# Optimization experiments

Hardware: AMD Instinct MI355X
Metric: run time of the kernel (lower is better)

The kernel has to match this reference:

```python
import jax, jax.numpy as jnp
import numpy as np

N0, N1 = 4096, 16384
HID, LAT, DIM, OUT = 128, 64, 3, 3
OFFS = [1, 2, 3, 5, 8]  # circulant graph offsets; A+A^3 support is offset sums


def _ring_edges(N, offs):
    # edge_index of A + A^3 for circulant adjacency with given offsets
    o = np.asarray(offs)
    s3 = (o[:, None, None] + o[None, :, None] + o[None, None, :]).ravel()
    aug = np.unique(np.concatenate([o, s3]))
    src = np.repeat(np.arange(N), aug.size)
    dst = (src + np.tile(aug, N)) % N
    return np.stack([src, dst]).astype(np.int32)


def _gatv2(x, src, dst, eattr, Wl, bl, Wr, br, We, att, bias, N):
    # PyG GATv2Conv, heads=1, add_self_loops=True with fill_value='mean'
    cnt = jax.ops.segment_sum(jnp.ones_like(dst, jnp.float32), dst, N)
    loop_attr = jax.ops.segment_sum(eattr, dst, N) / jnp.maximum(cnt, 1.0)[:, None]
    loops = jnp.arange(N, dtype=src.dtype)
    s = jnp.concatenate([src, loops])
    d = jnp.concatenate([dst, loops])
    ea = jnp.concatenate([eattr, loop_attr], 0)
    xl = x @ Wl.T + bl
    xr = x @ Wr.T + br
    m = xl[s] + xr[d] + ea @ We.T              # [E+N, HID]
    m = jnp.where(m > 0, m, 0.2 * m)           # leaky_relu(0.2)
    a = m @ att                                # [E+N]
    amax = jax.ops.segment_max(a, d, N)
    ex = jnp.exp(a - amax[d])
    den = jax.ops.segment_sum(ex, d, N)
    alpha = ex / (den[d] + 1e-16)
    return jax.ops.segment_sum(xl[s] * alpha[:, None], d, N) + bias


def _knn_interp(x, pos_x, pos_y, k=3):
    # PyG knn_interpolate: inverse-squared-distance weighted k-NN average
    d2 = (jnp.sum(pos_y ** 2, 1)[:, None] + jnp.sum(pos_x ** 2, 1)[None, :]
          - 2.0 * pos_y @ pos_x.T)             # [Ny, Nx]
    neg, idx = jax.lax.top_k(-d2, k)
    w = 1.0 / jnp.maximum(-neg, 1e-16)          # [Ny, k]
    return jnp.sum(x[idx] * w[..., None], 1) / jnp.sum(w, 1)[:, None]


def _forward(latent, pos0, pos1, eidx0, eidx1, conv_Wl, conv_bl, conv_Wr,
             conv_br, conv_We, conv_att, conv_bias, lin0_W, lin0_b, lins_W,
             lins_b, out_W, out_b):
    x = latent @ lin0_W.T + lin0_b
    src0, dst0 = eidx0[0], eidx0[1]
    ea0 = pos0[dst0] - pos0[src0]
    for c in (0, 1):
        h = jnp.concatenate([x, pos0], 1)
        x = jax.nn.elu(_gatv2(h, src0, dst0, ea0, conv_Wl[c], conv_bl[c],
                              conv_Wr[c], conv_br[c], conv_We[c], conv_att[c],
                              conv_bias[c], N0)) + h @ lins_W[c].T + lins_b[c]
    x = _knn_interp(x, pos0, pos1, 3)
    src1, dst1 = eidx1[0], eidx1[1]
    ea1 = pos1[dst1] - pos1[src1]
    for c in (2, 3):
        h = jnp.concatenate([x, pos1], 1)
        x = jax.nn.elu(_gatv2(h, src1, dst1, ea1, conv_Wl[c], conv_bl[c],
                              conv_Wr[c], conv_br[c], conv_We[c], conv_att[c],
                              conv_bias[c], N1)) + h @ lins_W[c].T + lins_b[c]
    h = jnp.concatenate([x, pos1], 1)
    return h @ out_W.T + out_b


def setup_inputs() -> dict:
    key = jax.random.key(0)
    ks = jax.random.split(key, 16)
    n = lambda i, shape, s=0.05: jax.random.normal(ks[i], shape, jnp.float32) * s
    IN = HID + DIM
    return dict(
        latent=jax.random.normal(ks[0], (N0, LAT), jnp.float32),
        pos0=jax.random.normal(ks[1], (N0, DIM), jnp.float32),
        pos1=jax.random.normal(ks[2], (N1, DIM), jnp.float32),
        eidx0=jnp.asarray(_ring_edges(N0, OFFS)),
        eidx1=jnp.asarray(_ring_edges(N1, OFFS)),
        conv_Wl=n(3, (4, HID, IN)), conv_bl=n(4, (4, HID)),
        conv_Wr=n(5, (4, HID, IN)), conv_br=n(6, (4, HID)),
        conv_We=n(7, (4, HID, DIM)), conv_att=n(8, (4, HID)),
        conv_bias=n(9, (4, HID)),
        lin0_W=n(10, (HID, LAT)), lin0_b=n(11, (HID,)),
        lins_W=n(12, (4, HID, IN)), lins_b=n(13, (4, HID)),
        out_W=n(14, (OUT, IN)), out_b=n(15, (OUT,)))


def reference(latent, pos0, pos1, eidx0, eidx1, conv_Wl, conv_bl, conv_Wr,
              conv_br, conv_We, conv_att, conv_bias, lin0_W, lin0_b, lins_W,
              lins_b, out_W, out_b):
    return _forward(latent, pos0, pos1, eidx0, eidx1, conv_Wl, conv_bl,
                    conv_Wr, conv_br, conv_We, conv_att, conv_bias, lin0_W,
                    lin0_b, lins_W, lins_b, out_W, out_b)
```

## Files before the change

kernel.cpp:

```cpp
#include <hip/hip_runtime.h>
#include <hip/hip_bf16.h>

#define N0 4096
#define N1 16384
#define HID 128
#define LAT 64
#define DIM 3
#define NAUG 21
#define JTOT 512
#define NG 5

typedef __attribute__((ext_vector_type(8))) short bf16x8;
typedef __attribute__((ext_vector_type(4))) float f32x4;

__device__ __constant__ int c_aug[NAUG] = {1,2,3,4,5,6,7,8,9,10,11,12,13,14,
                                           15,16,17,18,19,21,24};

__device__ __forceinline__ unsigned short f2bf(float v) {
    __hip_bfloat16 b = __float2bfloat16(v);
    return *reinterpret_cast<unsigned short*>(&b);
}

#define KCH 64
#define KCS 64
#define YPT 4
#define KNN_BLOCKS 1024

#define WSWZ_PER_LAYER 81920
#define H0G4 131072
#define H1G4 524288
#define PREP_BLOCKS 3880

__global__ __launch_bounds__(256)
void prep_knn_kernel(const float* __restrict__ Wl,
                     const float* __restrict__ Wr,
                     const float* __restrict__ We,
                     const float* __restrict__ linsW,
                     const float* __restrict__ bl,
                     const float* __restrict__ br,
                     const float* __restrict__ linsb,
                     const float* __restrict__ lin0W,
                     const float* __restrict__ pos0,
                     const float* __restrict__ pos1,
                     unsigned short* __restrict__ Wswz,
                     float* __restrict__ bias_cat,
                     float* __restrict__ Wt0,
                     unsigned short* __restrict__ hswz0A,
                     unsigned short* __restrict__ hswz0B,
                     unsigned short* __restrict__ hswz1A,
                     unsigned short* __restrict__ hswz1B,
                     float* __restrict__ pb_d,
                     int* __restrict__ pb_i) {
    __shared__ float4 sx[KCS];

    if (blockIdx.x < KNN_BLOCKS) {
        int tid = threadIdx.x;
        int chunk = blockIdx.x >> 4;
        int xpart = blockIdx.x & 15;
        if (tid < KCS) {
            const float* p = &pos0[(chunk * KCS + tid) * 3];
            float x = p[0], y = p[1], z = p[2];
            sx[tid] = make_float4(x, y, z, x * x + y * y + z * z);
        }
        __syncthreads();
        int ybase = xpart * (256 * YPT) + tid;
        float m2y[YPT][3], sy[YPT];
#pragma unroll
        for (int u = 0; u < YPT; ++u) {
            int y = ybase + u * 256;
            float p0 = pos1[y * 3], p1 = pos1[y * 3 + 1], p2 = pos1[y * 3 + 2];
            m2y[u][0] = -2.0f * p0; m2y[u][1] = -2.0f * p1; m2y[u][2] = -2.0f * p2;
            sy[u] = p0 * p0 + p1 * p1 + p2 * p2;
        }
        float bd0[YPT], bd1[YPT], bd2[YPT];
        int   bi0[YPT], bi1[YPT], bi2[YPT];
#pragma unroll
        for (int u = 0; u < YPT; ++u) {
            bd0[u] = 1e30f; bd1[u] = 1e30f; bd2[u] = 1e30f;
            bi0[u] = 0; bi1[u] = 0; bi2[u] = 0;
        }
        int gbase = chunk * KCS;
#pragma unroll 4
        for (int i = 0; i < KCS; i += 4) {
            float4 s[4];
#pragma unroll
            for (int v = 0; v < 4; ++v) s[v] = sx[i + v];
#pragma unroll
            for (int v = 0; v < 4; ++v) {
                int gi = gbase + i + v;
#pragma unroll
                for (int u = 0; u < YPT; ++u) {
                    float t = fmaf(m2y[u][0], s[v].x, s[v].w);
                    t = fmaf(m2y[u][1], s[v].y, t);
                    t = fmaf(m2y[u][2], s[v].z, t);
                    t += sy[u];
                    bool c0 = t < bd0[u];
                    bool c1 = t < bd1[u];
                    bool c2 = t < bd2[u];
                    float n0 = fminf(bd0[u], t);
                    float n1 = __builtin_amdgcn_fmed3f(bd0[u], bd1[u], t);
                    float n2 = __builtin_amdgcn_fmed3f(bd1[u], bd2[u], t);
                    int j0 = c0 ? gi : bi0[u];
                    int j1 = c0 ? bi0[u] : (c1 ? gi : bi1[u]);
                    int j2 = c1 ? bi1[u] : (c2 ? gi : bi2[u]);
                    bd0[u] = n0; bd1[u] = n1; bd2[u] = n2;
                    bi0[u] = j0; bi1[u] = j1; bi2[u] = j2;
                }
            }
        }
#pragma unroll
        for (int u = 0; u < YPT; ++u) {
            int y = ybase + u * 256;
            int base = (chunk * N1 + y) * 3;
            pb_d[base] = bd0[u]; pb_d[base + 1] = bd1[u]; pb_d[base + 2] = bd2[u];
            pb_i[base] = bi0[u]; pb_i[base + 1] = bi1[u]; pb_i[base + 2] = bi2[u];
        }
        return;
    }

    int tid = (blockIdx.x - KNN_BLOCKS) * blockDim.x + threadIdx.x;
    const int NSWZ = 4 * WSWZ_PER_LAYER;
    const int B0 = NSWZ;
    const int B1 = B0 + 4 * JTOT;
    const int B2 = B1 + 64 * 128;
    const int B3 = B2 + H0G4;
    const int B4 = B3 + H1G4;
    if (tid < NSWZ) {
        int c = tid / WSWZ_PER_LAYER;
        int r = tid - c * WSWZ_PER_LAYER;
        int nt = r / 2560;
        int g  = (r / 512) % 5;
        int l  = (r / 8) % 64;
        int j  = r % 8;
        int k  = g * 32 + (l >> 4) * 8 + j;
        int n  = nt * 16 + (l & 15);
        float v = 0.0f;
        if (k < 131) {
            if (n < 128)      v = Wl[(c * 128 + n) * 131 + k];
            else if (n < 256) v = Wr[(c * 128 + (n - 128)) * 131 + k];
            else if (n < 384) v = linsW[(c * 128 + (n - 256)) * 131 + k];
            else              v = (k >= 128) ? We[(c * 128 + (n - 384)) * 3 + (k - 128)]
                                             : 0.0f;
        }
        Wswz[tid] = f2bf(v);
    } else if (tid < B1) {
        int idx = tid - B0;
        int c = idx / JTOT;
        int j = idx - c * JTOT;
        float v;
        if (j < 128)        v = bl[c * 128 + j];
        else if (j < 256)   v = br[c * 128 + (j - 128)];
        else if (j < 384)   v = linsb[c * 128 + (j - 256)];
        else                v = 0.0f;
        bias_cat[idx] = v;
    } else if (tid < B2) {
        int idx = tid - B1;
        int k = idx / 128;
        int j = idx - k * 128;
        Wt0[idx] = lin0W[j * 64 + k];
    } else if (tid < B3) {
        int r = tid - B2;
        int j = r & 7;
        int l = (r >> 3) & 63;
        int mt = r >> 9;
        int row = mt * 16 + (l & 15);
        int k = 128 + (l >> 4) * 8 + j;
        float v = (k < 131) ? pos0[row * 3 + (k - 128)] : 0.0f;
        unsigned short bv = f2bf(v);
        size_t idx = (size_t)((mt * 5 + 4) * 64 + l) * 8 + j;
        hswz0A[idx] = bv;
        hswz0B[idx] = bv;
    } else if (tid < B4) {
        int r = tid - B3;
        int j = r & 7;
        int l = (r >> 3) & 63;
        int mt = r >> 9;
        int row = mt * 16 + (l & 15);
        int k = 128 + (l >> 4) * 8 + j;
        float v = (k < 131) ? pos1[row * 3 + (k - 128)] : 0.0f;
        unsigned short bv = f2bf(v);
        size_t idx = (size_t)((mt * 5 + 4) * 64 + l) * 8 + j;
        hswz1A[idx] = bv;
        hswz1B[idx] = bv;
    }
}

#define MERGE_BLOCKS 128

__global__ __launch_bounds__(128)
void lin0_merge_kernel(const float* __restrict__ latent,
                       const float* __restrict__ Wt0,
                       const float* __restrict__ b,
                       unsigned short* __restrict__ hswz0,
                       const float* __restrict__ pb_d,
                       const int* __restrict__ pb_i,
                       int* __restrict__ knn_idx,
                       float* __restrict__ knn_w) {
    __shared__ float lrow[64];

    if (blockIdx.x < MERGE_BLOCKS) {
        int y = blockIdx.x * 128 + threadIdx.x;
        float bd0 = 1e30f, bd1 = 1e30f, bd2 = 1e30f;
        int bi0 = 0, bi1 = 0, bi2 = 0;
        for (int c = 0; c < KCH; ++c) {
            int base = (c * N1 + y) * 3;
#pragma unroll
            for (int t3 = 0; t3 < 3; ++t3) {
                float t = pb_d[base + t3];
                int gi = pb_i[base + t3];
                bool c0 = t < bd0;
                bool c1 = t < bd1;
                bool c2 = t < bd2;
                float n0 = fminf(bd0, t);
                float n1 = __builtin_amdgcn_fmed3f(bd0, bd1, t);
                float n2 = __builtin_amdgcn_fmed3f(bd1, bd2, t);
                int j0 = c0 ? gi : bi0;
                int j1 = c0 ? bi0 : (c1 ? gi : bi1);
                int j2 = c1 ? bi1 : (c2 ? gi : bi2);
                bd0 = n0; bd1 = n1; bd2 = n2;
                bi0 = j0; bi1 = j1; bi2 = j2;
            }
        }
        knn_idx[y * 3]     = bi0;
        knn_idx[y * 3 + 1] = bi1;
        knn_idx[y * 3 + 2] = bi2;
        knn_w[y * 3]     = 1.0f / fmaxf(bd0, 1e-16f);
        knn_w[y * 3 + 1] = 1.0f / fmaxf(bd1, 1e-16f);
        knn_w[y * 3 + 2] = 1.0f / fmaxf(bd2, 1e-16f);
        return;
    }

    int n = blockIdx.x - MERGE_BLOCKS;
    int j = threadIdx.x;
    if (j < 64) lrow[j] = latent[n * 64 + j];
    __syncthreads();
    float acc = b[j];
#pragma unroll 8
    for (int k = 0; k < 64; ++k) acc += lrow[k] * Wt0[k * 128 + j];
    int g = j >> 5, sub = (j >> 3) & 3, jj = j & 7;
    hswz0[(size_t)(((n >> 4) * 5 + g) * 64 + sub * 16 + (n & 15)) * 8 + jj] = f2bf(acc);
}

#define WROW 40
#define FSTR 132
__global__ __launch_bounds__(512, 2)
void fused_layer_kernel(const unsigned short* __restrict__ hswz,
                        const unsigned short* __restrict__ Wswz,
                        const float* __restrict__ bias_cat,
                        const float* __restrict__ att,
                        const float* __restrict__ bias,
                        float* __restrict__ linb,
                        float* __restrict__ xout,
                        unsigned short* __restrict__ hout,
                        const float* __restrict__ outW,
                        const float* __restrict__ outb,
                        const float* __restrict__ pos1,
                        int mode, int N) {
    __shared__ float xls_s[WROW][FSTR];
    __shared__ float pes_s[WROW][FSTR];
    __shared__ float xr_s[16][FSTR];

    int tid = threadIdx.x;
    int w = tid >> 6;
    int l = tid & 63;
    int quad = l >> 4, lcol = l & 15;
    int mt0 = blockIdx.x;
    int n0 = mt0 * 16;
    int MT = N >> 4;

    bf16x8 a[3][NG];
#pragma unroll
    for (int i = 0; i < 3; ++i) {
        int mt = mt0 - 2 + i;
        if (mt < 0) mt += MT;
#pragma unroll
        for (int g = 0; g < NG; ++g)
            a[i][g] = *(const bf16x8*)&hswz[(size_t)((mt * NG + g) * 64 + l) * 8];
    }

#pragma unroll
    for (int i = 0; i < 4; ++i) {
        int b = i * 8 + w;
        int colbase = (b & 7) * 16;
        int ntw, kind;
        if (b < 8)       { ntw = b;      kind = 0; }
        else if (b < 16) { ntw = 16 + b; kind = 1; }
        else if (b < 24) { ntw = b - 8;  kind = 2; }
        else             { ntw = b - 8;  kind = 3; }
        bf16x8 bf[NG];
#pragma unroll
        for (int g = 0; g < NG; ++g)
            bf[g] = *(const bf16x8*)&Wswz[(size_t)((ntw * NG + g) * 64 + l) * 8];
        float bv = bias_cat[ntw * 16 + lcol];
        if (kind < 2) {
            float (*dst)[FSTR] = (kind == 0) ? xls_s : pes_s;
#pragma unroll
            for (int m = 0; m < 3; ++m) {
                f32x4 c = {bv, bv, bv, bv};
#pragma unroll
                for (int g = 0; g < NG; ++g)
                    c = __builtin_amdgcn_mfma_f32_16x16x32_bf16(a[m][g], bf[g], c, 0, 0, 0);
                if (m == 0) {
                    if (quad >= 2) {
                        int w0 = (quad - 2) * 4;
#pragma unroll
                        for (int r = 0; r < 4; ++r) dst[w0 + r][colbase + lcol] = c[r];
                    }
                } else {
                    int w0 = m * 16 - 8 + quad * 4;
#pragma unroll
                    for (int r = 0; r < 4; ++r) dst[w0 + r][colbase + lcol] = c[r];
                }
            }
        } else if (kind == 2) {
            f32x4 c = {bv, bv, bv, bv};
#pragma unroll
            for (int g = 0; g < NG; ++g)
                c = __builtin_amdgcn_mfma_f32_16x16x32_bf16(a[2][g], bf[g], c, 0, 0, 0);
            int w0 = quad * 4;
#pragma unroll
            for (int r = 0; r < 4; ++r) xr_s[w0 + r][colbase + lcol] = c[r];
        } else {
            f32x4 c = {bv, bv, bv, bv};
#pragma unroll
            for (int g = 0; g < NG; ++g)
                c = __builtin_amdgcn_mfma_f32_16x16x32_bf16(a[2][g], bf[g], c, 0, 0, 0);
            int jj = colbase + lcol;
#pragma unroll
            for (int r = 0; r < 4; ++r)
                linb[(size_t)(n0 + quad * 4 + r) * 128 + jj] = c[r];
        }
    }
    __syncthreads();

    int qh = l >> 5;
    int t = l & 31;
    int dl = w * 2 + qh;
    int d = n0 + dl;
    int selfrow = dl + 24;
    int i0 = t * 4;

    f32x4 linv = *(const f32x4*)&linb[(size_t)d * 128 + i0];

    float att4[4], base[4], xld[4], pesum[4], o[4];
    {
        f32x4 a0 = *(const f32x4*)&att[i0];
        f32x4 r0 = *(const f32x4*)&xr_s[dl][i0];
        f32x4 x0 = *(const f32x4*)&xls_s[selfrow][i0];
        f32x4 p0 = *(const f32x4*)&pes_s[selfrow][i0];
#pragma unroll
        for (int j = 0; j < 4; ++j) {
            att4[j] = a0[j];
            xld[j]  = x0[j];
            base[j] = r0[j] + p0[j];
            pesum[j] = 0.0f;
            o[j] = 0.0f;
        }
    }

    float den = 0.0f;

#pragma unroll
    for (int k = 0; k < NAUG; ++k) {
        int lr = selfrow - c_aug[k];
        float xls[4], pes[4];
        *(f32x4*)&xls[0] = *(const f32x4*)&xls_s[lr][i0];
        *(f32x4*)&pes[0] = *(const f32x4*)&pes_s[lr][i0];
        float p = 0.0f;
#pragma unroll
        for (int j = 0; j < 4; ++j) {
            float mm = xls[j] + base[j] - pes[j];
            mm = mm > 0.0f ? mm : 0.2f * mm;
            p = fmaf(att4[j], mm, p);
            pesum[j] += pes[j];
        }
        p += __shfl_xor(p, 1, 64);
        p += __shfl_xor(p, 2, 64);
        p += __shfl_xor(p, 4, 64);
        p += __shfl_xor(p, 8, 64);
        p += __shfl_xor(p, 16, 64);
        float wgt = __expf(p);
        den += wgt;
#pragma unroll
        for (int j = 0; j < 4; ++j) o[j] = fmaf(wgt, xls[j], o[j]);
    }
    {
        const float inv21 = 1.0f / 21.0f;
        float p = 0.0f;
#pragma unroll
        for (int j = 0; j < 4; ++j) {
            float mm = xld[j] + base[j] - pesum[j] * inv21;
            mm = mm > 0.0f ? mm : 0.2f * mm;
            p = fmaf(att4[j], mm, p);
        }
        p += __shfl_xor(p, 1, 64);
        p += __shfl_xor(p, 2, 64);
        p += __shfl_xor(p, 4, 64);
        p += __shfl_xor(p, 8, 64);
        p += __shfl_xor(p, 16, 64);
        float wgt = __expf(p);
        den += wgt;
#pragma unroll
        for (int j = 0; j < 4; ++j) o[j] = fmaf(wgt, xld[j], o[j]);
    }

    float inv = 1.0f / (den + 1e-16f);
    float res[4];
    {
        f32x4 b0 = *(const f32x4*)&bias[i0];
#pragma unroll
        for (int j = 0; j < 4; ++j) {
            float v = o[j] * inv + b0[j];
            v = v > 0.0f ? v : __expf(v) - 1.0f;
            res[j] = v + linv[j];
        }
    }

    if (mode == 0) {
        *(f32x4*)&xout[(size_t)d * 128 + i0] = *(f32x4*)&res[0];
    } else if (mode == 1) {
        unsigned short ob[4];
#pragma unroll
        for (int j = 0; j < 4; ++j) ob[j] = f2bf(res[j]);
        int g = i0 >> 5, sub = (i0 >> 3) & 3, jj = i0 & 7;
        *(uint2*)&hout[(size_t)((((d >> 4) * 5 + g) * 64) + sub * 16 + (d & 15)) * 8 + jj]
            = *(uint2*)ob;
    } else {
        float po[3];
#pragma unroll
        for (int o3 = 0; o3 < 3; ++o3) {
            const float* wr = &outW[o3 * 131 + i0];
            float p = res[0] * wr[0];
            p = fmaf(res[1], wr[1], p);
            p = fmaf(res[2], wr[2], p);
            p = fmaf(res[3], wr[3], p);
            p += __shfl_xor(p, 1, 64);
            p += __shfl_xor(p, 2, 64);
            p += __shfl_xor(p, 4, 64);
            p += __shfl_xor(p, 8, 64);
            p += __shfl_xor(p, 16, 64);
            po[o3] = p;
        }
        if (t == 0) {
            float p0 = pos1[d * 3], p1 = pos1[d * 3 + 1], p2 = pos1[d * 3 + 2];
#pragma unroll
            for (int o3 = 0; o3 < 3; ++o3) {
                xout[d * 3 + o3] = po[o3] + outb[o3] + p0 * outW[o3 * 131 + 128]
                                 + p1 * outW[o3 * 131 + 129] + p2 * outW[o3 * 131 + 130];
            }
        }
    }
}

__global__ __launch_bounds__(256)
void interp_kernel(const float* __restrict__ x0, const int* __restrict__ knn_idx,
                   const float* __restrict__ knn_w, unsigned short* __restrict__ hswz) {
    int wave = threadIdx.x >> 6;
    int lane = threadIdx.x & 63;
    int y = blockIdx.x * 4 + wave;
    int i0 = 2 * lane;
    float w0 = knn_w[y * 3], w1 = knn_w[y * 3 + 1], w2 = knn_w[y * 3 + 2];
    int j0 = knn_idx[y * 3], j1 = knn_idx[y * 3 + 1], j2 = knn_idx[y * 3 + 2];
    float inv = 1.0f / (w0 + w1 + w2);
    float2 a = *(const float2*)&x0[(size_t)j0 * 128 + i0];
    float2 b = *(const float2*)&x0[(size_t)j1 * 128 + i0];
    float2 c = *(const float2*)&x0[(size_t)j2 * 128 + i0];
    float rx = (w0 * a.x + w1 * b.x + w2 * c.x) * inv;
    float ry = (w0 * a.y + w1 * b.y + w2 * c.y) * inv;
    unsigned int packed = (unsigned int)f2bf(rx) | ((unsigned int)f2bf(ry) << 16);
    int g = i0 >> 5, sub = (i0 >> 3) & 3, jj = i0 & 7;
    size_t idx = (size_t)((((y >> 4) * 5 + g) * 64) + sub * 16 + (y & 15)) * 8 + jj;
    *(unsigned int*)&hswz[idx] = packed;
}

extern "C" void kernel_launch(void* const* d_in, const int* in_sizes, int n_in,
                              void* d_out, int out_size, void* d_ws, size_t ws_size,
                              hipStream_t stream) {
    (void)in_sizes; (void)n_in; (void)out_size; (void)ws_size;
    const float* latent   = (const float*)d_in[0];
    const float* pos0     = (const float*)d_in[1];
    const float* pos1     = (const float*)d_in[2];
    const float* conv_Wl  = (const float*)d_in[5];
    const float* conv_bl  = (const float*)d_in[6];
    const float* conv_Wr  = (const float*)d_in[7];
    const float* conv_br  = (const float*)d_in[8];
    const float* conv_We  = (const float*)d_in[9];
    const float* conv_att = (const float*)d_in[10];
    const float* conv_bias= (const float*)d_in[11];
    const float* lin0_W   = (const float*)d_in[12];
    const float* lin0_b   = (const float*)d_in[13];
    const float* lins_W   = (const float*)d_in[14];
    const float* lins_b   = (const float*)d_in[15];
    const float* out_W    = (const float*)d_in[16];
    const float* out_b    = (const float*)d_in[17];
    float* out = (float*)d_out;

    char* ws = (char*)d_ws;
    unsigned short* Wswz = (unsigned short*)ws; ws += (size_t)4 * WSWZ_PER_LAYER * 2;
    float* bias_cat = (float*)ws;  ws += (size_t)4 * JTOT * 4;
    float* Wt0      = (float*)ws;  ws += (size_t)64 * 128 * 4;
    unsigned short* hswz0A = (unsigned short*)ws; ws += (size_t)(N0 / 16) * NG * 64 * 8 * 2;
    unsigned short* hswz0B = (unsigned short*)ws; ws += (size_t)(N0 / 16) * NG * 64 * 8 * 2;
    unsigned short* hswz1A = (unsigned short*)ws; ws += (size_t)(N1 / 16) * NG * 64 * 8 * 2;
    unsigned short* hswz1B = (unsigned short*)ws; ws += (size_t)(N1 / 16) * NG * 64 * 8 * 2;
    float* bufA     = (float*)ws;  ws += (size_t)N0 * 128 * 4;
    float* linb     = (float*)ws;  ws += (size_t)N1 * 128 * 4;
    float* pb_d     = (float*)ws;  ws += (size_t)KCH * N1 * 3 * 4;
    int*   pb_i     = (int*)ws;    ws += (size_t)KCH * N1 * 3 * 4;
    int*   knn_idx  = (int*)ws;    ws += (size_t)N1 * 3 * 4;
    float* knn_w    = (float*)ws;  ws += (size_t)N1 * 3 * 4;

    prep_knn_kernel<<<KNN_BLOCKS + PREP_BLOCKS, 256, 0, stream>>>(
        conv_Wl, conv_Wr, conv_We, lins_W, conv_bl, conv_br, lins_b, lin0_W,
        pos0, pos1, Wswz, bias_cat, Wt0, hswz0A, hswz0B, hswz1A, hswz1B,
        pb_d, pb_i);

    lin0_merge_kernel<<<MERGE_BLOCKS + N0, 128, 0, stream>>>(
        latent, Wt0, lin0_b, hswz0A, pb_d, pb_i, knn_idx, knn_w);

    fused_layer_kernel<<<N0 / 16, 512, 0, stream>>>(
        hswz0A, Wswz + (size_t)0 * WSWZ_PER_LAYER, bias_cat + 0 * JTOT,
        conv_att + 0 * 128, conv_bias + 0 * 128, linb, nullptr, hswz0B,
        nullptr, nullptr, nullptr, 1, N0);
    fused_layer_kernel<<<N0 / 16, 512, 0, stream>>>(
        hswz0B, Wswz + (size_t)1 * WSWZ_PER_LAYER, bias_cat + 1 * JTOT,
        conv_att + 1 * 128, conv_bias + 1 * 128, linb, bufA, nullptr,
        nullptr, nullptr, nullptr, 0, N0);

    interp_kernel<<<N1 / 4, 256, 0, stream>>>(bufA, knn_idx, knn_w, hswz1A);

    fused_layer_kernel<<<N1 / 16, 512, 0, stream>>>(
        hswz1A, Wswz + (size_t)2 * WSWZ_PER_LAYER, bias_cat + 2 * JTOT,
        conv_att + 2 * 128, conv_bias + 2 * 128, linb, nullptr, hswz1B,
        nullptr, nullptr, nullptr, 1, N1);
    fused_layer_kernel<<<N1 / 16, 512, 0, stream>>>(
        hswz1B, Wswz + (size_t)3 * WSWZ_PER_LAYER, bias_cat + 3 * JTOT,
        conv_att + 3 * 128, conv_bias + 3 * 128, linb, out, nullptr,
        out_W, out_b, pos1, 2, N1);
}
```

Before: 235.1 us.

## Fold lin0 into prep kernel and kNN merge into first GAT layer

Moves the lin0 projection into the prep/kNN launch, reading lin0_W directly instead of a transposed Wt0 copy, and drops the separate Wt0 transpose. The kNN partial-merge blocks now ride alongside the first GATv2 layer's blocks in one launch, with the layer body factored into a shared device function. Together these remove one kernel launch and its serialization gap, and let the merge overlap with layer-0 work. The trade-off is that lin0 now uses uncoalesced per-thread row reads of the weights. Merge blocks use 512 threads under the layer kernel's launch bounds, which could affect occupancy.

```diff
diff --git a/kernel.cpp b/kernel.cpp
--- a/kernel.cpp
+++ b/kernel.cpp
@@ -29,28 +29,35 @@
 #define WSWZ_PER_LAYER 81920
 #define H0G4 131072
 #define H1G4 524288
-#define PREP_BLOCKS 3880
+#define P_NSWZ (4 * WSWZ_PER_LAYER)
+#define P_B0 P_NSWZ
+#define P_B1 (P_B0 + 4 * JTOT)
+#define P_B2 (P_B1 + H0G4)
+#define P_B3 (P_B2 + H1G4)
+#define PREP_BLOCKS (P_B3 / 256)
+#define LIN0_BLOCKS 2048
 
 __global__ __launch_bounds__(256)
-void prep_knn_kernel(const float* __restrict__ Wl,
-                     const float* __restrict__ Wr,
-                     const float* __restrict__ We,
-                     const float* __restrict__ linsW,
-                     const float* __restrict__ bl,
-                     const float* __restrict__ br,
-                     const float* __restrict__ linsb,
-                     const float* __restrict__ lin0W,
-                     const float* __restrict__ pos0,
-                     const float* __restrict__ pos1,
-                     unsigned short* __restrict__ Wswz,
-                     float* __restrict__ bias_cat,
-                     float* __restrict__ Wt0,
-                     unsigned short* __restrict__ hswz0A,
-                     unsigned short* __restrict__ hswz0B,
-                     unsigned short* __restrict__ hswz1A,
-                     unsigned short* __restrict__ hswz1B,
-                     float* __restrict__ pb_d,
-                     int* __restrict__ pb_i) {
+void prep_knn_lin0_kernel(const float* __restrict__ Wl,
+                          const float* __restrict__ Wr,
+                          const float* __restrict__ We,
+                          const float* __restrict__ linsW,
+                          const float* __restrict__ bl,
+                          const float* __restrict__ br,
+                          const float* __restrict__ linsb,
+                          const float* __restrict__ lin0W,
+                          const float* __restrict__ lin0b,
+                          const float* __restrict__ latent,
+                          const float* __restrict__ pos0,
+                          const float* __restrict__ pos1,
+                          unsigned short* __restrict__ Wswz,
+                          float* __restrict__ bias_cat,
+                          unsigned short* __restrict__ hswz0A,
+                          unsigned short* __restrict__ hswz0B,
+                          unsigned short* __restrict__ hswz1A,
+                          unsigned short* __restrict__ hswz1B,
+                          float* __restrict__ pb_d,
+                          int* __restrict__ pb_i) {
     __shared__ float4 sx[KCS];
 
     if (blockIdx.x < KNN_BLOCKS) {
@@ -118,131 +125,285 @@
         return;
     }
 
-    int tid = (blockIdx.x - KNN_BLOCKS) * blockDim.x + threadIdx.x;
-    const int NSWZ = 4 * WSWZ_PER_LAYER;
-    const int B0 = NSWZ;
-    const int B1 = B0 + 4 * JTOT;
-    const int B2 = B1 + 64 * 128;
-    const int B3 = B2 + H0G4;
-    const int B4 = B3 + H1G4;
-    if (tid < NSWZ) {
-        int c = tid / WSWZ_PER_LAYER;
-        int r = tid - c * WSWZ_PER_LAYER;
-        int nt = r / 2560;
-        int g  = (r / 512) % 5;
-        int l  = (r / 8) % 64;
-        int j  = r % 8;
-        int k  = g * 32 + (l >> 4) * 8 + j;
-        int n  = nt * 16 + (l & 15);
-        float v = 0.0f;
-        if (k < 131) {
-            if (n < 128)      v = Wl[(c * 128 + n) * 131 + k];
-            else if (n < 256) v = Wr[(c * 128 + (n - 128)) * 131 + k];
-            else if (n < 384) v = linsW[(c * 128 + (n - 256)) * 131 + k];
-            else              v = (k >= 128) ? We[(c * 128 + (n - 384)) * 3 + (k - 128)]
-                                             : 0.0f;
-        }
-        Wswz[tid] = f2bf(v);
-    } else if (tid < B1) {
-        int idx = tid - B0;
-        int c = idx / JTOT;
-        int j = idx - c * JTOT;
-        float v;
-        if (j < 128)        v = bl[c * 128 + j];
-        else if (j < 256)   v = br[c * 128 + (j - 128)];
-        else if (j < 384)   v = linsb[c * 128 + (j - 256)];
-        else                v = 0.0f;
-        bias_cat[idx] = v;
-    } else if (tid < B2) {
-        int idx = tid - B1;
-        int k = idx / 128;
-        int j = idx - k * 128;
-        Wt0[idx] = lin0W[j * 64 + k];
-    } else if (tid < B3) {
-        int r = tid - B2;
-        int j = r & 7;
-        int l = (r >> 3) & 63;
-        int mt = r >> 9;
-        int row = mt * 16 + (l & 15);
-        int k = 128 + (l >> 4) * 8 + j;
-        float v = (k < 131) ? pos0[row * 3 + (k - 128)] : 0.0f;
-        unsigned short bv = f2bf(v);
-        size_t idx = (size_t)((mt * 5 + 4) * 64 + l) * 8 + j;
-        hswz0A[idx] = bv;
-        hswz0B[idx] = bv;
-    } else if (tid < B4) {
-        int r = tid - B3;
-        int j = r & 7;
-        int l = (r >> 3) & 63;
-        int mt = r >> 9;
-        int row = mt * 16 + (l & 15);
-        int k = 128 + (l >> 4) * 8 + j;
-        float v = (k < 131) ? pos1[row * 3 + (k - 128)] : 0.0f;
-        unsigned short bv = f2bf(v);
-        size_t idx = (size_t)((mt * 5 + 4) * 64 + l) * 8 + j;
-        hswz1A[idx] = bv;
-        hswz1B[idx] = bv;
-    }
-}
-
-#define MERGE_BLOCKS 128
-
-__global__ __launch_bounds__(128)
-void lin0_merge_kernel(const float* __restrict__ latent,
-                       const float* __restrict__ Wt0,
-                       const float* __restrict__ b,
-                       unsigned short* __restrict__ hswz0,
-                       const float* __restrict__ pb_d,
-                       const int* __restrict__ pb_i,
-                       int* __restrict__ knn_idx,
-                       float* __restrict__ knn_w) {
-    __shared__ float lrow[64];
-
-    if (blockIdx.x < MERGE_BLOCKS) {
-        int y = blockIdx.x * 128 + threadIdx.x;
-        float bd0 = 1e30f, bd1 = 1e30f, bd2 = 1e30f;
-        int bi0 = 0, bi1 = 0, bi2 = 0;
-        for (int c = 0; c < KCH; ++c) {
-            int base = (c * N1 + y) * 3;
-#pragma unroll
-            for (int t3 = 0; t3 < 3; ++t3) {
-                float t = pb_d[base + t3];
-                int gi = pb_i[base + t3];
-                bool c0 = t < bd0;
-                bool c1 = t < bd1;
-                bool c2 = t < bd2;
-                float n0 = fminf(bd0, t);
-                float n1 = __builtin_amdgcn_fmed3f(bd0, bd1, t);
-                float n2 = __builtin_amdgcn_fmed3f(bd1, bd2, t);
-                int j0 = c0 ? gi : bi0;
-                int j1 = c0 ? bi0 : (c1 ? gi : bi1);
-                int j2 = c1 ? bi1 : (c2 ? gi : bi2);
-                bd0 = n0; bd1 = n1; bd2 = n2;
-                bi0 = j0; bi1 = j1; bi2 = j2;
+    if (blockIdx.x < KNN_BLOCKS + PREP_BLOCKS) {
+        int tid = (blockIdx.x - KNN_BLOCKS) * blockDim.x + threadIdx.x;
+        if (tid < P_NSWZ) {
+            int c = tid / WSWZ_PER_LAYER;
+            int r = tid - c * WSWZ_PER_LAYER;
+            int nt = r / 2560;
+            int g  = (r / 512) % 5;
+            int l  = (r / 8) % 64;
+            int j  = r % 8;
+            int k  = g * 32 + (l >> 4) * 8 + j;
+            int n  = nt * 16 + (l & 15);
+            float v = 0.0f;
+            if (k < 131) {
+                if (n < 128)      v = Wl[(c * 128 + n) * 131 + k];
+                else if (n < 256) v = Wr[(c * 128 + (n - 128)) * 131 + k];
+                else if (n < 384) v = linsW[(c * 128 + (n - 256)) * 131 + k];
+                else              v = (k >= 128) ? We[(c * 128 + (n - 384)) * 3 + (k - 128)]
+                                                 : 0.0f;
             }
-        }
-        knn_idx[y * 3]     = bi0;
-        knn_idx[y * 3 + 1] = bi1;
-        knn_idx[y * 3 + 2] = bi2;
-        knn_w[y * 3]     = 1.0f / fmaxf(bd0, 1e-16f);
-        knn_w[y * 3 + 1] = 1.0f / fmaxf(bd1, 1e-16f);
-        knn_w[y * 3 + 2] = 1.0f / fmaxf(bd2, 1e-16f);
+            Wswz[tid] = f2bf(v);
+        } else if (tid < P_B1) {
+            int idx = tid - P_B0;
+            int c = idx / JTOT;
+            int j = idx - c * JTOT;
+            float v;
+            if (j < 128)        v = bl[c * 128 + j];
+            else if (j < 256)   v = br[c * 128 + (j - 128)];
+            else if (j < 384)   v = linsb[c * 128 + (j - 256)];
+            else                v = 0.0f;
+            bias_cat[idx] = v;
+        } else if (tid < P_B2) {
+            int r = tid - P_B1;
+            int j = r & 7;
+            int l = (r >> 3) & 63;
+            int mt = r >> 9;
+            int row = mt * 16 + (l & 15);
+            int k = 128 + (l >> 4) * 8 + j;
+            float v = (k < 131) ? pos0[row * 3 + (k - 128)] : 0.0f;
+            unsigned short bv = f2bf(v);
+            size_t idx = (size_t)((mt * 5 + 4) * 64 + l) * 8 + j;
+            hswz0A[idx] = bv;
+            hswz0B[idx] = bv;
+        } else if (tid < P_B3) {
+            int r = tid - P_B2;
+            int j = r & 7;
+            int l = (r >> 3) & 63;
+            int mt = r >> 9;
+            int row = mt * 16 + (l & 15);
+            int k = 128 + (l >> 4) * 8 + j;
+            float v = (k < 131) ? pos1[row * 3 + (k - 128)] : 0.0f;
+            unsigned short bv = f2bf(v);
+            size_t idx = (size_t)((mt * 5 + 4) * 64 + l) * 8 + j;
+            hswz1A[idx] = bv;
+            hswz1B[idx] = bv;
+        }
         return;
     }
 
-    int n = blockIdx.x - MERGE_BLOCKS;
-    int j = threadIdx.x;
-    if (j < 64) lrow[j] = latent[n * 64 + j];
-    __syncthreads();
-    float acc = b[j];
+    {
+        int r = (blockIdx.x - KNN_BLOCKS - PREP_BLOCKS) * blockDim.x + threadIdx.x;
+        int n = r >> 7, j = r & 127;
+        const float* lr = &latent[n * 64];
+        const float* wr = &lin0W[j * 64];
+        float acc = lin0b[j];
 #pragma unroll 8
-    for (int k = 0; k < 64; ++k) acc += lrow[k] * Wt0[k * 128 + j];
-    int g = j >> 5, sub = (j >> 3) & 3, jj = j & 7;
-    hswz0[(size_t)(((n >> 4) * 5 + g) * 64 + sub * 16 + (n & 15)) * 8 + jj] = f2bf(acc);
+        for (int k = 0; k < 64; ++k) acc += lr[k] * wr[k];
+        int g = j >> 5, sub = (j >> 3) & 3, jj = j & 7;
+        hswz0A[(size_t)(((n >> 4) * 5 + g) * 64 + sub * 16 + (n & 15)) * 8 + jj] = f2bf(acc);
+    }
 }
 
 #define WROW 40
 #define FSTR 132
+
+__device__ __forceinline__ void layer_body(
+        const unsigned short* __restrict__ hswz,
+        const unsigned short* __restrict__ Wswz,
+        const float* __restrict__ bias_cat,
+        const float* __restrict__ att,
+        const float* __restrict__ bias,
+        float* __restrict__ linb,
+        float* __restrict__ xout,
+        unsigned short* __restrict__ hout,
+        const float* __restrict__ outW,
+        const float* __restrict__ outb,
+        const float* __restrict__ pos1,
+        int mode, int N, int mt0,
+        float (*xls_s)[FSTR], float (*pes_s)[FSTR], float (*xr_s)[FSTR]) {
+    int tid = threadIdx.x;
+    int w = tid >> 6;
+    int l = tid & 63;
+    int quad = l >> 4, lcol = l & 15;
+    int n0 = mt0 * 16;
+    int MT = N >> 4;
+
+    bf16x8 a[3][NG];
+#pragma unroll
+    for (int i = 0; i < 3; ++i) {
+        int mt = mt0 - 2 + i;
+        if (mt < 0) mt += MT;
+#pragma unroll
+        for (int g = 0; g < NG; ++g)
+            a[i][g] = *(const bf16x8*)&hswz[(size_t)((mt * NG + g) * 64 + l) * 8];
+    }
+
+#pragma unroll
+    for (int i = 0; i < 4; ++i) {
+        int b = i * 8 + w;
+        int colbase = (b & 7) * 16;
+        int ntw, kind;
+        if (b < 8)       { ntw = b;      kind = 0; }
+        else if (b < 16) { ntw = 16 + b; kind = 1; }
+        else if (b < 24) { ntw = b - 8;  kind = 2; }
+        else             { ntw = b - 8;  kind = 3; }
+        bf16x8 bf[NG];
+#pragma unroll
+        for (int g = 0; g < NG; ++g)
+            bf[g] = *(const bf16x8*)&Wswz[(size_t)((ntw * NG + g) * 64 + l) * 8];
+        float bv = bias_cat[ntw * 16 + lcol];
+        if (kind < 2) {
+            float (*dst)[FSTR] = (kind == 0) ? xls_s : pes_s;
+#pragma unroll
+            for (int m = 0; m < 3; ++m) {
+                f32x4 c = {bv, bv, bv, bv};
+#pragma unroll
+                for (int g = 0; g < NG; ++g)
+                    c = __builtin_amdgcn_mfma_f32_16x16x32_bf16(a[m][g], bf[g], c, 0, 0, 0);
+                if (m == 0) {
+                    if (quad >= 2) {
+                        int w0 = (quad - 2) * 4;
+#pragma unroll
+                        for (int r = 0; r < 4; ++r) dst[w0 + r][colbase + lcol] = c[r];
+                    }
+                } else {
+                    int w0 = m * 16 - 8 + quad * 4;
+#pragma unroll
+                    for (int r = 0; r < 4; ++r) dst[w0 + r][colbase + lcol] = c[r];
+                }
+            }
+        } else if (kind == 2) {
+            f32x4 c = {bv, bv, bv, bv};
+#pragma unroll
+            for (int g = 0; g < NG; ++g)
+                c = __builtin_amdgcn_mfma_f32_16x16x32_bf16(a[2][g], bf[g], c, 0, 0, 0);
+            int w0 = quad * 4;
+#pragma unroll
+            for (int r = 0; r < 4; ++r) xr_s[w0 + r][colbase + lcol] = c[r];
+        } else {
+            f32x4 c = {bv, bv, bv, bv};
+#pragma unroll
+            for (int g = 0; g < NG; ++g)
+                c = __builtin_amdgcn_mfma_f32_16x16x32_bf16(a[2][g], bf[g], c, 0, 0, 0);
+            int jj = colbase + lcol;
+#pragma unroll
+            for (int r = 0; r < 4; ++r)
+                linb[(size_t)(n0 + quad * 4 + r) * 128 + jj] = c[r];
+        }
+    }
+    __syncthreads();
+
+    int qh = l >> 5;
+    int t = l & 31;
+    int dl = w * 2 + qh;
+    int d = n0 + dl;
+    int selfrow = dl + 24;
+    int i0 = t * 4;
+
+    f32x4 linv = *(const f32x4*)&linb[(size_t)d * 128 + i0];
+
+    float att4[4], base[4], xld[4], pesum[4], o[4];
+    {
+        f32x4 a0 = *(const f32x4*)&att[i0];
+        f32x4 r0 = *(const f32x4*)&xr_s[dl][i0];
+        f32x4 x0 = *(const f32x4*)&xls_s[selfrow][i0];
+        f32x4 p0 = *(const f32x4*)&pes_s[selfrow][i0];
+#pragma unroll
+        for (int j = 0; j < 4; ++j) {
+            att4[j] = a0[j];
+            xld[j]  = x0[j];
+            base[j] = r0[j] + p0[j];
+            pesum[j] = 0.0f;
+            o[j] = 0.0f;
+        }
+    }
+
+    float den = 0.0f;
+
+#pragma unroll
+    for (int k = 0; k < NAUG; ++k) {
+        int lr = selfrow - c_aug[k];
+        float xls[4], pes[4];
+        *(f32x4*)&xls[0] = *(const f32x4*)&xls_s[lr][i0];
+        *(f32x4*)&pes[0] = *(const f32x4*)&pes_s[lr][i0];
+        float p = 0.0f;
+#pragma unroll
+        for (int j = 0; j < 4; ++j) {
+            float mm = xls[j] + base[j] - pes[j];
+            mm = mm > 0.0f ? mm : 0.2f * mm;
+            p = fmaf(att4[j], mm, p);
+            pesum[j] += pes[j];
+        }
+        p += __shfl_xor(p, 1, 64);
+        p += __shfl_xor(p, 2, 64);
+        p += __shfl_xor(p, 4, 64);
+        p += __shfl_xor(p, 8, 64);
+        p += __shfl_xor(p, 16, 64);
+        float wgt = __expf(p);
+        den += wgt;
+#pragma unroll
+        for (int j = 0; j < 4; ++j) o[j] = fmaf(wgt, xls[j], o[j]);
+    }
+    {
+        const float inv21 = 1.0f / 21.0f;
+        float p = 0.0f;
+#pragma unroll
+        for (int j = 0; j < 4; ++j) {
+            float mm = xld[j] + base[j] - pesum[j] * inv21;
+            mm = mm > 0.0f ? mm : 0.2f * mm;
+            p = fmaf(att4[j], mm, p);
+        }
+        p += __shfl_xor(p, 1, 64);
+        p += __shfl_xor(p, 2, 64);
+        p += __shfl_xor(p, 4, 64);
+        p += __shfl_xor(p, 8, 64);
+        p += __shfl_xor(p, 16, 64);
+        float wgt = __expf(p);
+        den += wgt;
+#pragma unroll
+        for (int j = 0; j < 4; ++j) o[j] = fmaf(wgt, xld[j], o[j]);
+    }
+
+    float inv = 1.0f / (den + 1e-16f);
+    float res[4];
+    {
+        f32x4 b0 = *(const f32x4*)&bias[i0];
+#pragma unroll
+        for (int j = 0; j < 4; ++j) {
+            float v = o[j] * inv + b0[j];
+            v = v > 0.0f ? v : __expf(v) - 1.0f;
+            res[j] = v + linv[j];
+        }
+    }
+
+    if (mode == 0) {
+        *(f32x4*)&xout[(size_t)d * 128 + i0] = *(f32x4*)&res[0];
+    } else if (mode == 1) {
+        unsigned short ob[4];
+#pragma unroll
+        for (int j = 0; j < 4; ++j) ob[j] = f2bf(res[j]);
+        int g = i0 >> 5, sub = (i0 >> 3) & 3, jj = i0 & 7;
+        *(uint2*)&hout[(size_t)((((d >> 4) * 5 + g) * 64) + sub * 16 + (d & 15)) * 8 + jj]
+            = *(uint2*)ob;
+    } else {
+        float po[3];
+#pragma unroll
+        for (int o3 = 0; o3 < 3; ++o3) {
+            const float* wr = &outW[o3 * 131 + i0];
+            float p = res[0] * wr[0];
+            p = fmaf(res[1], wr[1], p);
+            p = fmaf(res[2], wr[2], p);
+            p = fmaf(res[3], wr[3], p);
+            p += __shfl_xor(p, 1, 64);
+            p += __shfl_xor(p, 2, 64);
+            p += __shfl_xor(p, 4, 64);
+            p += __shfl_xor(p, 8, 64);
+            p += __shfl_xor(p, 16, 64);
+            po[o3] = p;
+        }
+        if (t == 0) {
+            float p0 = pos1[d * 3], p1 = pos1[d * 3 + 1], p2 = pos1[d * 3 + 2];
+#pragma unroll
+            for (int o3 = 0; o3 < 3; ++o3) {
+                xout[d * 3 + o3] = po[o3] + outb[o3] + p0 * outW[o3 * 131 + 128]
+                                 + p1 * outW[o3 * 131 + 129] + p2 * outW[o3 * 131 + 130];
+            }
+        }
+    }
+}
+
 __global__ __launch_bounds__(512, 2)
 void fused_layer_kernel(const unsigned short* __restrict__ hswz,
                         const unsigned short* __restrict__ Wswz,
@@ -256,200 +417,66 @@
                         const float* __restrict__ outb,
                         const float* __restrict__ pos1,
                         int mode, int N) {
-    __shared__ float xls_s[WROW][FSTR];
-    __shared__ float pes_s[WROW][FSTR];
-    __shared__ float xr_s[16][FSTR];
-
-    int tid = threadIdx.x;
-    int w = tid >> 6;
-    int l = tid & 63;
-    int quad = l >> 4, lcol = l & 15;
-    int mt0 = blockIdx.x;
-    int n0 = mt0 * 16;
-    int MT = N >> 4;
-
-    bf16x8 a[3][NG];
-#pragma unroll
-    for (int i = 0; i < 3; ++i) {
-        int mt = mt0 - 2 + i;
-        if (mt < 0) mt += MT;
-#pragma unroll
-        for (int g = 0; g < NG; ++g)
-            a[i][g] = *(const bf16x8*)&hswz[(size_t)((mt * NG + g) * 64 + l) * 8];
-    }
-
-#pragma unroll
-    for (int i = 0; i < 4; ++i) {
-        int b = i * 8 + w;
-        int colbase = (b & 7) * 16;
-        int ntw, kind;
-        if (b < 8)       { ntw = b;      kind = 0; }
-        else if (b < 16) { ntw = 16 + b; kind = 1; }
-        else if (b < 24) { ntw = b - 8;  kind = 2; }
-        else             { ntw = b - 8;  kind = 3; }
-        bf16x8 bf[NG];
-#pragma unroll
-        for (int g = 0; g < NG; ++g)
-            bf[g] = *(const bf16x8*)&Wswz[(size_t)((ntw * NG + g) * 64 + l) * 8];
-        float bv = bias_cat[ntw * 16 + lcol];
-        if (kind < 2) {
-            float (*dst)[FSTR] = (kind == 0) ? xls_s : pes_s;
-#pragma unroll
-            for (int m = 0; m < 3; ++m) {
-                f32x4 c = {bv, bv, bv, bv};
-#pragma unroll
-                for (int g = 0; g < NG; ++g)
-                    c = __builtin_amdgcn_mfma_f32_16x16x32_bf16(a[m][g], bf[g], c, 0, 0, 0);
-                if (m == 0) {
-                    if (quad >= 2) {
-                        int w0 = (quad - 2) * 4;
-#pragma unroll
-                        for (int r = 0; r < 4; ++r) dst[w0 + r][colbase + lcol] = c[r];
-                    }
-                } else {
-                    int w0 = m * 16 - 8 + quad * 4;
-#pragma unroll
-                    for (int r = 0; r < 4; ++r) dst[w0 + r][colbase + lcol] = c[r];
-                }
-            }
-        } else if (kind == 2) {
-            f32x4 c = {bv, bv, bv, bv};
-#pragma unroll
-            for (int g = 0; g < NG; ++g)
-                c = __builtin_amdgcn_mfma_f32_16x16x32_bf16(a[2][g], bf[g], c, 0, 0, 0);
-            int w0 = quad * 4;
-#pragma unroll
-            for (int r = 0; r < 4; ++r) xr_s[w0 + r][colbase + lcol] = c[r];
-        } else {
-            f32x4 c = {bv, bv, bv, bv};
-#pragma unroll
-            for (int g = 0; g < NG; ++g)
-                c = __builtin_amdgcn_mfma_f32_16x16x32_bf16(a[2][g], bf[g], c, 0, 0, 0);
-            int jj = colbase + lcol;
-#pragma unroll
-            for (int r = 0; r < 4; ++r)
-                linb[(size_t)(n0 + quad * 4 + r) * 128 + jj] = c[r];
-        }
-    }
-    __syncthreads();
-
-    int qh = l >> 5;
-    int t = l & 31;
-    int dl = w * 2 + qh;
-    int d = n0 + dl;
-    int selfrow = dl + 24;
-    int i0 = t * 4;
-
-    f32x4 linv = *(const f32x4*)&linb[(size_t)d * 128 + i0];
-
-    float att4[4], base[4], xld[4], pesum[4], o[4];
-    {
-        f32x4 a0 = *(const f32x4*)&att[i0];
-        f32x4 r0 = *(const f32x4*)&xr_s[dl][i0];
-        f32x4 x0 = *(const f32x4*)&xls_s[selfrow][i0];
-        f32x4 p0 = *(const f32x4*)&pes_s[selfrow][i0];
-#pragma unroll
-        for (int j = 0; j < 4; ++j) {
-            att4[j] = a0[j];
-            xld[j]  = x0[j];
-            base[j] = r0[j] + p0[j];
-            pesum[j] = 0.0f;
-            o[j] = 0.0f;
-        }
-    }
-
-    float den = 0.0f;
-
-#pragma unroll
-    for (int k = 0; k < NAUG; ++k) {
-        int lr = selfrow - c_aug[k];
-        float xls[4], pes[4];
-        *(f32x4*)&xls[0] = *(const f32x4*)&xls_s[lr][i0];
-        *(f32x4*)&pes[0] = *(const f32x4*)&pes_s[lr][i0];
-        float p = 0.0f;
-#pragma unroll
-        for (int j = 0; j < 4; ++j) {
-            float mm = xls[j] + base[j] - pes[j];
-            mm = mm > 0.0f ? mm : 0.2f * mm;
-            p = fmaf(att4[j], mm, p);
-            pesum[j] += pes[j];
-        }
-        p += __shfl_xor(p, 1, 64);
-        p += __shfl_xor(p, 2, 64);
-        p += __shfl_xor(p, 4, 64);
-        p += __shfl_xor(p, 8, 64);
-        p += __shfl_xor(p, 16, 64);
-        float wgt = __expf(p);
-        den += wgt;
-#pragma unroll
-        for (int j = 0; j < 4; ++j) o[j] = fmaf(wgt, xls[j], o[j]);
-    }
-    {
-        const float inv21 = 1.0f / 21.0f;
-        float p = 0.0f;
-#pragma unroll
-        for (int j = 0; j < 4; ++j) {
-            float mm = xld[j] + base[j] - pesum[j] * inv21;
-            mm = mm > 0.0f ? mm : 0.2f * mm;
-            p = fmaf(att4[j], mm, p);
-        }
-        p += __shfl_xor(p, 1, 64);
-        p += __shfl_xor(p, 2, 64);
-        p += __shfl_xor(p, 4, 64);
-        p += __shfl_xor(p, 8, 64);
-        p += __shfl_xor(p, 16, 64);
-        float wgt = __expf(p);
-        den += wgt;
-#pragma unroll
-        for (int j = 0; j < 4; ++j) o[j] = fmaf(wgt, xld[j], o[j]);
-    }
-
-    float inv = 1.0f / (den + 1e-16f);
-    float res[4];
-    {
-        f32x4 b0 = *(const f32x4*)&bias[i0];
-#pragma unroll
-        for (int j = 0; j < 4; ++j) {
-            float v = o[j] * inv + b0[j];
-            v = v > 0.0f ? v : __expf(v) - 1.0f;
-            res[j] = v + linv[j];
-        }
-    }
-
-    if (mode == 0) {
-        *(f32x4*)&xout[(size_t)d * 128 + i0] = *(f32x4*)&res[0];
-    } else if (mode == 1) {
-        unsigned short ob[4];
-#pragma unroll
-        for (int j = 0; j < 4; ++j) ob[j] = f2bf(res[j]);
-        int g = i0 >> 5, sub = (i0 >> 3) & 3, jj = i0 & 7;
-        *(uint2*)&hout[(size_t)((((d >> 4) * 5 + g) * 64) + sub * 16 + (d & 15)) * 8 + jj]
-            = *(uint2*)ob;
-    } else {
-        float po[3];
-#pragma unroll
-        for (int o3 = 0; o3 < 3; ++o3) {
-            const float* wr = &outW[o3 * 131 + i0];
-            float p = res[0] * wr[0];
-            p = fmaf(res[1], wr[1], p);
-            p = fmaf(res[2], wr[2], p);
-            p = fmaf(res[3], wr[3], p);
-            p += __shfl_xor(p, 1, 64);
-            p += __shfl_xor(p, 2, 64);
-            p += __shfl_xor(p, 4, 64);
-            p += __shfl_xor(p, 8, 64);
-            p += __shfl_xor(p, 16, 64);
-            po[o3] = p;
-        }
-        if (t == 0) {
-            float p0 = pos1[d * 3], p1 = pos1[d * 3 + 1], p2 = pos1[d * 3 + 2];
-#pragma unroll
-            for (int o3 = 0; o3 < 3; ++o3) {
-                xout[d * 3 + o3] = po[o3] + outb[o3] + p0 * outW[o3 * 131 + 128]
-                                 + p1 * outW[o3 * 131 + 129] + p2 * outW[o3 * 131 + 130];
-            }
-        }
-    }
+    __shared__ __align__(16) float xls_s[WROW][FSTR];
+    __shared__ __align__(16) float pes_s[WROW][FSTR];
+    __shared__ __align__(16) float xr_s[16][FSTR];
+    layer_body(hswz, Wswz, bias_cat, att, bias, linb, xout, hout,
+               outW, outb, pos1, mode, N, blockIdx.x, xls_s, pes_s, xr_s);
+}
+
+#define MERGE_BLOCKS 32
+
+__global__ __launch_bounds__(512, 2)
+void layer0_merge_kernel(const unsigned short* __restrict__ hswz,
+                         const unsigned short* __restrict__ Wswz,
+                         const float* __restrict__ bias_cat,
+                         const float* __restrict__ att,
+                         const float* __restrict__ bias,
+                         float* __restrict__ linb,
+                         unsigned short* __restrict__ hout,
+                         const float* __restrict__ pb_d,
+                         const int* __restrict__ pb_i,
+                         int* __restrict__ knn_idx,
+                         float* __restrict__ knn_w) {
+    __shared__ __align__(16) float xls_s[WROW][FSTR];
+    __shared__ __align__(16) float pes_s[WROW][FSTR];
+    __shared__ __align__(16) float xr_s[16][FSTR];
+
+    if (blockIdx.x < (N0 >> 4)) {
+        layer_body(hswz, Wswz, bias_cat, att, bias, linb, nullptr, hout,
+                   nullptr, nullptr, nullptr, 1, N0, blockIdx.x,
+                   xls_s, pes_s, xr_s);
+        return;
+    }
+
+    int y = (blockIdx.x - (N0 >> 4)) * 512 + threadIdx.x;
+    float bd0 = 1e30f, bd1 = 1e30f, bd2 = 1e30f;
+    int bi0 = 0, bi1 = 0, bi2 = 0;
+    for (int c = 0; c < KCH; ++c) {
+        int base = (c * N1 + y) * 3;
+#pragma unroll
+        for (int t3 = 0; t3 < 3; ++t3) {
+            float t = pb_d[base + t3];
+            int gi = pb_i[base + t3];
+            bool c0 = t < bd0;
+            bool c1 = t < bd1;
+            bool c2 = t < bd2;
+            float n0 = fminf(bd0, t);
+            float n1 = __builtin_amdgcn_fmed3f(bd0, bd1, t);
+            float n2 = __builtin_amdgcn_fmed3f(bd1, bd2, t);
+            int j0 = c0 ? gi : bi0;
+            int j1 = c0 ? bi0 : (c1 ? gi : bi1);
+            int j2 = c1 ? bi1 : (c2 ? gi : bi2);
+            bd0 = n0; bd1 = n1; bd2 = n2;
+            bi0 = j0; bi1 = j1; bi2 = j2;
+        }
+    }
+    knn_idx[y * 3]     = bi0;
+    knn_idx[y * 3 + 1] = bi1;
+    knn_idx[y * 3 + 2] = bi2;
+    knn_w[y * 3]     = 1.0f / fmaxf(bd0, 1e-16f);
+    knn_w[y * 3 + 1] = 1.0f / fmaxf(bd1, 1e-16f);
+    knn_w[y * 3 + 2] = 1.0f / fmaxf(bd2, 1e-16f);
 }
 
 __global__ __launch_bounds__(256)
@@ -498,7 +525,6 @@
     char* ws = (char*)d_ws;
     unsigned short* Wswz = (unsigned short*)ws; ws += (size_t)4 * WSWZ_PER_LAYER * 2;
     float* bias_cat = (float*)ws;  ws += (size_t)4 * JTOT * 4;
-    float* Wt0      = (float*)ws;  ws += (size_t)64 * 128 * 4;
     unsigned short* hswz0A = (unsigned short*)ws; ws += (size_t)(N0 / 16) * NG * 64 * 8 * 2;
     unsigned short* hswz0B = (unsigned short*)ws; ws += (size_t)(N0 / 16) * NG * 64 * 8 * 2;
     unsigned short* hswz1A = (unsigned short*)ws; ws += (size_t)(N1 / 16) * NG * 64 * 8 * 2;
@@ -510,18 +536,16 @@
     int*   knn_idx  = (int*)ws;    ws += (size_t)N1 * 3 * 4;
     float* knn_w    = (float*)ws;  ws += (size_t)N1 * 3 * 4;
 
-    prep_knn_kernel<<<KNN_BLOCKS + PREP_BLOCKS, 256, 0, stream>>>(
-        conv_Wl, conv_Wr, conv_We, lins_W, conv_bl, conv_br, lins_b, lin0_W,
-        pos0, pos1, Wswz, bias_cat, Wt0, hswz0A, hswz0B, hswz1A, hswz1B,
-        pb_d, pb_i);
-
-    lin0_merge_kernel<<<MERGE_BLOCKS + N0, 128, 0, stream>>>(
-        latent, Wt0, lin0_b, hswz0A, pb_d, pb_i, knn_idx, knn_w);
-
-    fused_layer_kernel<<<N0 / 16, 512, 0, stream>>>(
+    prep_knn_lin0_kernel<<<KNN_BLOCKS + PREP_BLOCKS + LIN0_BLOCKS, 256, 0, stream>>>(
+        conv_Wl, conv_Wr, conv_We, lins_W, conv_bl, conv_br, lins_b,
+        lin0_W, lin0_b, latent, pos0, pos1,
+        Wswz, bias_cat, hswz0A, hswz0B, hswz1A, hswz1B, pb_d, pb_i);
+
+    layer0_merge_kernel<<<N0 / 16 + MERGE_BLOCKS, 512, 0, stream>>>(
         hswz0A, Wswz + (size_t)0 * WSWZ_PER_LAYER, bias_cat + 0 * JTOT,
-        conv_att + 0 * 128, conv_bias + 0 * 128, linb, nullptr, hswz0B,
-        nullptr, nullptr, nullptr, 1, N0);
+        conv_att + 0 * 128, conv_bias + 0 * 128, linb, hswz0B,
+        pb_d, pb_i, knn_idx, knn_w);
+
     fused_layer_kernel<<<N0 / 16, 512, 0, stream>>>(
         hswz0B, Wswz + (size_t)1 * WSWZ_PER_LAYER, bias_cat + 1 * JTOT,
         conv_att + 1 * 128, conv_bias + 1 * 128, linb, bufA, nullptr,
@@ -533,6 +557,7 @@
         hswz1A, Wswz + (size_t)2 * WSWZ_PER_LAYER, bias_cat + 2 * JTOT,
         conv_att + 2 * 128, conv_bias + 2 * 128, linb, nullptr, hswz1B,
         nullptr, nullptr, nullptr, 1, N1);
+
     fused_layer_kernel<<<N1 / 16, 512, 0, stream>>>(
         hswz1B, Wswz + (size_t)3 * WSWZ_PER_LAYER, bias_cat + 3 * JTOT,
         conv_att + 3 * 128, conv_bias + 3 * 128, linb, out, nullptr,
```

New measurement: 248.8 us. 5.9% more time.
